# Optimization experiments

Measured on AMD Instinct MI355X. Metric: run time of the kernel, lower is better.

## Reference

```python
import jax, jax.numpy as jnp
import numpy as np

N_NODES = 100000
NEG_SLOPE = 0.01  # torch F.leaky_relu default

def _degrees(edge_src, edge_dst, n):
    ones = jnp.ones(edge_src.shape[0], dtype=jnp.float32)
    dout = jax.ops.segment_sum(ones, edge_src, num_segments=n)
    din = jax.ops.segment_sum(ones, edge_dst, num_segments=n)
    # DGL clamps zero degrees to 1 (norm='both')
    dout_inv_sqrt = jax.lax.rsqrt(jnp.maximum(dout, 1.0))
    din_inv_sqrt = jax.lax.rsqrt(jnp.maximum(din, 1.0))
    return dout_inv_sqrt, din_inv_sqrt

def _graph_conv(x, W, b, edge_src, edge_dst, dout_is, din_is, n):
    # DGL GraphConv, norm='both': h_i = b + sum_{j->i} (x_j W) / sqrt(d_out(j) d_in(i))
    h = (x * dout_is[:, None]) @ W            # [N, out]
    agg = jax.ops.segment_sum(h[edge_src], edge_dst, num_segments=n)
    return agg * din_is[:, None] + b

def setup_inputs() -> dict:
    key = jax.random.key(0)
    ks = jax.random.split(key, 16)
    n, e = N_NODES, 1600000
    features = jax.random.normal(ks[0], (n, 4), dtype=jnp.float32)
    edge_src = jax.random.randint(ks[1], (e,), 0, n, dtype=jnp.int32)
    edge_dst = jax.random.randint(ks[2], (e,), 0, n, dtype=jnp.int32)
    dims = [(4, 128), (128, 128), (128, 128), (128, 128), (128, 3)]
    inp = {"features": features, "edge_src": edge_src, "edge_dst": edge_dst}
    for i, (fi, fo) in enumerate(dims):
        s = (2.0 / (fi + fo)) ** 0.5  # glorot
        inp[f"W{i+1}"] = jax.random.normal(ks[3 + i], (fi, fo), dtype=jnp.float32) * s
        inp[f"b{i+1}"] = jnp.zeros((fo,), dtype=jnp.float32)
    return inp

def reference(features, edge_src, edge_dst, W1, b1, W2, b2, W3, b3, W4, b4, W5, b5):
    n = features.shape[0]
    dout_is, din_is = _degrees(edge_src, edge_dst, n)
    lrelu = lambda x: jnp.where(x >= 0, x, NEG_SLOPE * x)
    x = lrelu(_graph_conv(features, W1, b1, edge_src, edge_dst, dout_is, din_is, n))
    x = lrelu(_graph_conv(x, W2, b2, edge_src, edge_dst, dout_is, din_is, n))
    x = lrelu(_graph_conv(x, W3, b3, edge_src, edge_dst, dout_is, din_is, n))
    x = lrelu(_graph_conv(x, W4, b4, edge_src, edge_dst, dout_is, din_is, n))
    x = _graph_conv(x, W5, b5, edge_src, edge_dst, dout_is, din_is, n)
    return x
```

## Files before the change

### kernel.cpp

```cpp
#include <hip/hip_runtime.h>
#include <hip/hip_fp16.h>
#include <math.h>


#define LRELU_SLOPE 0.01f
#define XPAD 129
#define MAXBUCK 512


__device__ inline void chunk_range(int E, int nchunks, int cid, int& lo, int& hi) {
    int chunk = (E + nchunks - 1) / nchunks;
    lo = cid * chunk;
    hi = min(E, lo + chunk);
}

__global__ __launch_bounds__(256) void k_part_hist2(const int* __restrict__ src, const int* __restrict__ dst,
                                                    int E, int nbuck,
                                                    unsigned* __restrict__ gHistS, unsigned* __restrict__ gHistD,
                                                    unsigned* __restrict__ blockBaseS, unsigned* __restrict__ blockBaseD) {
    __shared__ unsigned hs[MAXBUCK];
    __shared__ unsigned hd[MAXBUCK];
    for (int i = threadIdx.x; i < nbuck; i += 256) { hs[i] = 0u; hd[i] = 0u; }
    __syncthreads();
    int lo, hi;
    chunk_range(E, gridDim.x, blockIdx.x, lo, hi);
    for (int e = lo + threadIdx.x; e < hi; e += 256) {
        atomicAdd(&hs[src[e] >> 8], 1u);
        atomicAdd(&hd[dst[e] >> 8], 1u);
    }
    __syncthreads();
    for (int i = threadIdx.x; i < nbuck; i += 256) {
        blockBaseS[(size_t)blockIdx.x * nbuck + i] = atomicAdd(&gHistS[i], hs[i]);
        blockBaseD[(size_t)blockIdx.x * nbuck + i] = atomicAdd(&gHistD[i], hd[i]);
    }
}

__global__ __launch_bounds__(512) void k_part_scan(const unsigned* __restrict__ gHist, int nbuck,
                                                   unsigned* __restrict__ bucketStart,
                                                   unsigned* __restrict__ row_ptr_last, unsigned Eval) {
    __shared__ unsigned s[MAXBUCK];
    int t = threadIdx.x;
    s[t] = (t < nbuck) ? gHist[t] : 0u;
    __syncthreads();
    for (int off = 1; off < MAXBUCK; off <<= 1) {
        unsigned v = (t >= off) ? s[t - off] : 0u;
        __syncthreads();
        s[t] += v;
        __syncthreads();
    }
    if (t <= nbuck) bucketStart[t] = (t == 0) ? 0u : s[t - 1];
    if (t == 0 && row_ptr_last) *row_ptr_last = Eval;
}

__global__ __launch_bounds__(256) void k_part_scatter_both(const int* __restrict__ src, const int* __restrict__ dst,
                                                           int E, int nbuck,
                                                           const unsigned* __restrict__ bstartS,
                                                           const unsigned* __restrict__ bstartD,
                                                           const unsigned* __restrict__ blockBaseS,
                                                           const unsigned* __restrict__ blockBaseD,
                                                           int2* __restrict__ pairs, int* __restrict__ srcbuf) {
    __shared__ unsigned curS[MAXBUCK];
    __shared__ unsigned curD[MAXBUCK];
    for (int i = threadIdx.x; i < nbuck; i += 256) {
        curS[i] = bstartS[i] + blockBaseS[(size_t)blockIdx.x * nbuck + i];
        curD[i] = bstartD[i] + blockBaseD[(size_t)blockIdx.x * nbuck + i];
    }
    __syncthreads();
    int lo, hi;
    chunk_range(E, gridDim.x, blockIdx.x, lo, hi);
    for (int e = lo + threadIdx.x; e < hi; e += 256) {
        int s = src[e], d = dst[e];
        unsigned posD = atomicAdd(&curD[d >> 8], 1u);
        pairs[posD] = make_int2(s, d);
        unsigned posS = atomicAdd(&curS[s >> 8], 1u);
        srcbuf[posS] = s;
    }
}

__global__ __launch_bounds__(256) void k_bucket_csr(const int2* __restrict__ pairs,
                                                    const unsigned* __restrict__ bucketStart,
                                                    unsigned* __restrict__ row_ptr,
                                                    unsigned* __restrict__ din_cnt,
                                                    int* __restrict__ csr, int n) {
    __shared__ unsigned hist[256];
    __shared__ unsigned scanw[256];
    __shared__ unsigned cur[256];
    int b = blockIdx.x, t = threadIdx.x;
    unsigned beg = bucketStart[b], end = bucketStart[b + 1];
    hist[t] = 0u;
    __syncthreads();
    for (unsigned e = beg + t; e < end; e += 256)
        atomicAdd(&hist[pairs[e].y & 255], 1u);
    __syncthreads();
    scanw[t] = hist[t];
    __syncthreads();
    for (int off = 1; off < 256; off <<= 1) {
        unsigned u = (t >= off) ? scanw[t - off] : 0u;
        __syncthreads();
        scanw[t] += u;
        __syncthreads();
    }
    unsigned excl = scanw[t] - hist[t];
    int node = (b << 8) + t;
    if (node < n) {
        row_ptr[node] = beg + excl;
        din_cnt[node] = hist[t];
    }
    cur[t] = excl;
    __syncthreads();
    for (unsigned e = beg + t; e < end; e += 256) {
        int2 p = pairs[e];
        unsigned pos = beg + atomicAdd(&cur[p.y & 255], 1u);
        csr[pos] = p.x;
    }
}

__global__ __launch_bounds__(256) void k_bucket_cnt(const int* __restrict__ vals,
                                                    const unsigned* __restrict__ bucketStart,
                                                    unsigned* __restrict__ dout_cnt, int n) {
    __shared__ unsigned hist[256];
    int b = blockIdx.x, t = threadIdx.x;
    unsigned beg = bucketStart[b], end = bucketStart[b + 1];
    hist[t] = 0u;
    __syncthreads();
    for (unsigned e = beg + t; e < end; e += 256)
        atomicAdd(&hist[vals[e] & 255], 1u);
    __syncthreads();
    int node = (b << 8) + t;
    if (node < n) dout_cnt[node] = hist[t];
}

__global__ void k_invsqrt2(const unsigned* __restrict__ c0, float* __restrict__ i0,
                           const unsigned* __restrict__ c1, float* __restrict__ i1, int n) {
    int i = blockIdx.x * blockDim.x + threadIdx.x;
    if (i < n) {
        i0[i] = 1.0f / sqrtf(fmaxf((float)c0[i], 1.0f));
        i1[i] = 1.0f / sqrtf(fmaxf((float)c1[i], 1.0f));
    }
}


__global__ void k_prescale4(const float* __restrict__ x, const float* __restrict__ dout_is,
                            float* __restrict__ pf4, int n) {
    int i = blockIdx.x * blockDim.x + threadIdx.x;
    if (i >= n) return;
    float s = dout_is[i];
    float4 v = *reinterpret_cast<const float4*>(x + (size_t)i * 4);
    float4 o = {v.x * s, v.y * s, v.z * s, v.w * s};
    *reinterpret_cast<float4*>(pf4 + (size_t)i * 4) = o;
}

__global__ void k_gather4(const float* __restrict__ pf4, const int* __restrict__ csr,
                          const unsigned* __restrict__ row_ptr, const float* __restrict__ din_is,
                          const float* __restrict__ dout_is, float* __restrict__ a4, int n) {
    int i = blockIdx.x * blockDim.x + threadIdx.x;
    if (i >= n) return;
    unsigned beg = row_ptr[i], end = row_ptr[i + 1];
    float4 acc = {0.f, 0.f, 0.f, 0.f};
    unsigned e = beg;
    for (; e + 4 <= end; e += 4) {
        int s0 = csr[e], s1 = csr[e + 1], s2 = csr[e + 2], s3 = csr[e + 3];
        float4 v0 = *reinterpret_cast<const float4*>(pf4 + (size_t)s0 * 4);
        float4 v1 = *reinterpret_cast<const float4*>(pf4 + (size_t)s1 * 4);
        float4 v2 = *reinterpret_cast<const float4*>(pf4 + (size_t)s2 * 4);
        float4 v3 = *reinterpret_cast<const float4*>(pf4 + (size_t)s3 * 4);
        acc.x += (v0.x + v1.x) + (v2.x + v3.x);
        acc.y += (v0.y + v1.y) + (v2.y + v3.y);
        acc.z += (v0.z + v1.z) + (v2.z + v3.z);
        acc.w += (v0.w + v1.w) + (v2.w + v3.w);
    }
    for (; e < end; ++e) {
        int s = csr[e];
        float4 v = *reinterpret_cast<const float4*>(pf4 + (size_t)s * 4);
        acc.x += v.x; acc.y += v.y; acc.z += v.z; acc.w += v.w;
    }
    float sc = din_is[i] * dout_is[i];
    float4 o = {acc.x * sc, acc.y * sc, acc.z * sc, acc.w * sc};
    *reinterpret_cast<float4*>(a4 + (size_t)i * 4) = o;
}


__device__ inline void sth16(__half* p, const float* v) {
    __half2 hh[8];
#pragma unroll
    for (int q = 0; q < 8; ++q) hh[q] = __floats2half2_rn(v[2 * q], v[2 * q + 1]);
    const float4* f = reinterpret_cast<const float4*>(&hh[0]);
    *reinterpret_cast<float4*>(p) = f[0];
    *reinterpret_cast<float4*>(p + 8) = f[1];
}

__device__ inline void acc8(float* acc, uint4 u) {
    const __half2* h = reinterpret_cast<const __half2*>(&u);
#pragma unroll
    for (int q = 0; q < 4; ++q) {
        float2 f = __half22float2(h[q]);
        acc[2 * q] += f.x;
        acc[2 * q + 1] += f.y;
    }
}


__device__ inline float4 xp1_cols(float4 av, float ds, float4 wa, float4 wb, float4 wc, float4 wd, float4 bc) {
    float4 r;
    r.x = fmaf(av.x, wa.x, fmaf(av.y, wb.x, fmaf(av.z, wc.x, fmaf(av.w, wd.x, ds * bc.x))));
    r.y = fmaf(av.x, wa.y, fmaf(av.y, wb.y, fmaf(av.z, wc.y, fmaf(av.w, wd.y, ds * bc.y))));
    r.z = fmaf(av.x, wa.z, fmaf(av.y, wb.z, fmaf(av.z, wc.z, fmaf(av.w, wd.z, ds * bc.z))));
    r.w = fmaf(av.x, wa.w, fmaf(av.y, wb.w, fmaf(av.z, wc.w, fmaf(av.w, wd.w, ds * bc.w))));
    r.x = fmaxf(r.x, LRELU_SLOPE * r.x);
    r.y = fmaxf(r.y, LRELU_SLOPE * r.y);
    r.z = fmaxf(r.z, LRELU_SLOPE * r.z);
    r.w = fmaxf(r.w, LRELU_SLOPE * r.w);
    return r;
}

__global__ __launch_bounds__(512) void k_gl12(const float* __restrict__ a4,
                                              const float* __restrict__ dout_v,
                                              const int* __restrict__ csr,
                                              const unsigned* __restrict__ row_ptr,
                                              const float* __restrict__ din_is, const float* __restrict__ dout_is,
                                              const float* __restrict__ W1, const float* __restrict__ b1,
                                              const float* __restrict__ W2, const float* __restrict__ b2,
                                              __half* __restrict__ xh_out, int n) {
    __shared__ float xs[64 * XPAD];
    const int t = threadIdx.x;
    const int bbase = blockIdx.x * 64;
    const int wave = t >> 6;
    const int lane = t & 63;
    const int half = lane >> 5;
    const int j4 = (lane & 31) * 4;

    float4 wa = *reinterpret_cast<const float4*>(W1 + 0 * 128 + j4);
    float4 wb = *reinterpret_cast<const float4*>(W1 + 1 * 128 + j4);
    float4 wc = *reinterpret_cast<const float4*>(W1 + 2 * 128 + j4);
    float4 wd = *reinterpret_cast<const float4*>(W1 + 3 * 128 + j4);
    float4 bc = *reinterpret_cast<const float4*>(b1 + j4);

#pragma unroll
    for (int sweep = 0; sweep < 4; ++sweep) {
        int r = wave * 2 + half + sweep * 16;
        int node = bbase + r;
        float4 acc = {0.f, 0.f, 0.f, 0.f};
        if (node < n) {
            unsigned beg = row_ptr[node], end = row_ptr[node + 1];
            unsigned e = beg;
            for (; e + 4 <= end; e += 4) {
                int s0 = csr[e + 0], s1 = csr[e + 1], s2 = csr[e + 2], s3 = csr[e + 3];
                float4 a0 = *reinterpret_cast<const float4*>(a4 + (size_t)s0 * 4);
                float4 a1 = *reinterpret_cast<const float4*>(a4 + (size_t)s1 * 4);
                float4 a2 = *reinterpret_cast<const float4*>(a4 + (size_t)s2 * 4);
                float4 a3 = *reinterpret_cast<const float4*>(a4 + (size_t)s3 * 4);
                float d0 = dout_v[s0], d1 = dout_v[s1], d2 = dout_v[s2], d3 = dout_v[s3];
                float4 x0 = xp1_cols(a0, d0, wa, wb, wc, wd, bc);
                float4 x1 = xp1_cols(a1, d1, wa, wb, wc, wd, bc);
                float4 x2 = xp1_cols(a2, d2, wa, wb, wc, wd, bc);
                float4 x3 = xp1_cols(a3, d3, wa, wb, wc, wd, bc);
                acc.x += (x0.x + x1.x) + (x2.x + x3.x);
                acc.y += (x0.y + x1.y) + (x2.y + x3.y);
                acc.z += (x0.z + x1.z) + (x2.z + x3.z);
                acc.w += (x0.w + x1.w) + (x2.w + x3.w);
            }
            for (; e < end; ++e) {
                int s = csr[e];
                float4 av = *reinterpret_cast<const float4*>(a4 + (size_t)s * 4);
                float4 xv = xp1_cols(av, dout_v[s], wa, wb, wc, wd, bc);
                acc.x += xv.x; acc.y += xv.y; acc.z += xv.z; acc.w += xv.w;
            }
            float di = din_is[node];
            acc.x *= di; acc.y *= di; acc.z *= di; acc.w *= di;
        }
        float* d = xs + r * XPAD + j4;
        d[0] = acc.x; d[1] = acc.y; d[2] = acc.z; d[3] = acc.w;
    }
    __syncthreads();

    const int jg = __builtin_amdgcn_readfirstlane(wave) & 7;
    const int j0 = jg * 16;
    const float* Wj = W2 + j0;
    const float* xrow = xs + lane * XPAD;

    float acc[16];
#pragma unroll
    for (int q = 0; q < 16; ++q) acc[q] = 0.f;

#pragma unroll 2
    for (int k = 0; k < 128; k += 4) {
        float x0 = xrow[k + 0];
        float x1 = xrow[k + 1];
        float x2 = xrow[k + 2];
        float x3 = xrow[k + 3];
        const float* w0 = Wj + (size_t)k * 128;
#pragma unroll
        for (int q = 0; q < 16; ++q) {
            acc[q] += x0 * w0[q] + x1 * w0[128 + q] + x2 * w0[256 + q] + x3 * w0[384 + q];
        }
    }

    int node = bbase + lane;
    if (node < n) {
        float s = dout_is[node];
        float v[16];
#pragma unroll
        for (int q = 0; q < 16; ++q) {
            float u = acc[q] + b2[j0 + q];
            u = fmaxf(u, LRELU_SLOPE * u);
            v[q] = u * s;
        }
        sth16(xh_out + (size_t)node * 128 + j0, v);
    }
}


#define GATHER_FP16_TILE(XH)                                                           \
    for (int sweep = 0; sweep < 8; ++sweep) {                                          \
        int r = sweep * 8 + wave;                                                      \
        int node = bbase + r;                                                          \
        float acc[8];                                                                  \
        _Pragma("unroll") for (int q = 0; q < 8; ++q) acc[q] = 0.f;                    \
        float di = 0.f;                                                                \
        if (node < n) {                                                                \
            unsigned beg = row_ptr[node], end = row_ptr[node + 1];                     \
            unsigned e = beg;                                                          \
            for (; e + 16 <= end; e += 16) {                                           \
                int s0 = csr[e + 0 + sub2];                                            \
                int s1 = csr[e + 4 + sub2];                                            \
                int s2 = csr[e + 8 + sub2];                                            \
                int s3 = csr[e + 12 + sub2];                                           \
                uint4 u0 = *reinterpret_cast<const uint4*>(XH + (size_t)s0 * 128 + c8); \
                uint4 u1 = *reinterpret_cast<const uint4*>(XH + (size_t)s1 * 128 + c8); \
                uint4 u2 = *reinterpret_cast<const uint4*>(XH + (size_t)s2 * 128 + c8); \
                uint4 u3 = *reinterpret_cast<const uint4*>(XH + (size_t)s3 * 128 + c8); \
                acc8(acc, u0); acc8(acc, u1); acc8(acc, u2); acc8(acc, u3);            \
            }                                                                          \
            for (; e + 4 <= end; e += 4) {                                             \
                int s = csr[e + sub2];                                                 \
                acc8(acc, *reinterpret_cast<const uint4*>(XH + (size_t)s * 128 + c8)); \
            }                                                                          \
            int rem = (int)(end - e);                                                  \
            if (sub2 < rem) {                                                          \
                int s = csr[e + sub2];                                                 \
                acc8(acc, *reinterpret_cast<const uint4*>(XH + (size_t)s * 128 + c8)); \
            }                                                                          \
            di = din_is[node];                                                         \
        }                                                                              \
        _Pragma("unroll") for (int q = 0; q < 8; ++q) {                                \
            acc[q] += __shfl_xor(acc[q], 16, 64);                                      \
            acc[q] += __shfl_xor(acc[q], 32, 64);                                      \
        }                                                                              \
        if (sub2 == 0) {                                                               \
            float* d = xs + r * XPAD + c8;                                             \
            _Pragma("unroll") for (int q = 0; q < 8; ++q) d[q] = acc[q] * di;          \
        }                                                                              \
    }


__global__ __launch_bounds__(512) void k_gl128h(const __half* __restrict__ xh, const int* __restrict__ csr,
                                                const unsigned* __restrict__ row_ptr,
                                                const float* __restrict__ din_is, const float* __restrict__ dout_is,
                                                const float* __restrict__ W, const float* __restrict__ b,
                                                __half* __restrict__ xh_out, int n) {
    __shared__ float xs[64 * XPAD];
    const int t = threadIdx.x;
    const int bbase = blockIdx.x * 64;
    const int wave = t >> 6;
    const int lane = t & 63;
    const int sub2 = lane >> 4;
    const int c8 = (lane & 15) * 8;

    GATHER_FP16_TILE(xh)
    __syncthreads();

    const int jg = __builtin_amdgcn_readfirstlane(wave) & 7;
    const int j0 = jg * 16;
    const float* Wj = W + j0;
    const float* xrow = xs + lane * XPAD;

    float acc[16];
#pragma unroll
    for (int q = 0; q < 16; ++q) acc[q] = 0.f;

#pragma unroll 2
    for (int k = 0; k < 128; k += 4) {
        float x0 = xrow[k + 0];
        float x1 = xrow[k + 1];
        float x2 = xrow[k + 2];
        float x3 = xrow[k + 3];
        const float* w0 = Wj + (size_t)k * 128;
#pragma unroll
        for (int q = 0; q < 16; ++q) {
            acc[q] += x0 * w0[q] + x1 * w0[128 + q] + x2 * w0[256 + q] + x3 * w0[384 + q];
        }
    }

    int node = bbase + lane;
    if (node < n) {
        float s = dout_is[node];
        float v[16];
#pragma unroll
        for (int q = 0; q < 16; ++q) {
            float u = acc[q] + b[j0 + q];
            u = fmaxf(u, LRELU_SLOPE * u);
            v[q] = u * s;
        }
        sth16(xh_out + (size_t)node * 128 + j0, v);
    }
}


__global__ __launch_bounds__(512) void k_gl128f(const __half* __restrict__ xh, const int* __restrict__ csr,
                                                const unsigned* __restrict__ row_ptr,
                                                const float* __restrict__ din_is, const float* __restrict__ dout_is,
                                                const float* __restrict__ W, const float* __restrict__ b,
                                                const float* __restrict__ W5,
                                                float* __restrict__ h5, int n) {
    __shared__ float xs[64 * XPAD];
    const int t = threadIdx.x;
    const int bbase = blockIdx.x * 64;
    const int wave = t >> 6;
    const int lane = t & 63;
    const int sub2 = lane >> 4;
    const int c8 = (lane & 15) * 8;

    GATHER_FP16_TILE(xh)
    __syncthreads();

    const int jg = __builtin_amdgcn_readfirstlane(wave) & 7;
    const int j0 = jg * 16;
    const float* Wj = W + j0;
    const float* xrow = xs + lane * XPAD;

    float acc[16];
#pragma unroll
    for (int q = 0; q < 16; ++q) acc[q] = 0.f;

#pragma unroll 2
    for (int k = 0; k < 128; k += 4) {
        float x0 = xrow[k + 0];
        float x1 = xrow[k + 1];
        float x2 = xrow[k + 2];
        float x3 = xrow[k + 3];
        const float* w0 = Wj + (size_t)k * 128;
#pragma unroll
        for (int q = 0; q < 16; ++q) {
            acc[q] += x0 * w0[q] + x1 * w0[128 + q] + x2 * w0[256 + q] + x3 * w0[384 + q];
        }
    }

    float s = (bbase + lane < n) ? dout_is[bbase + lane] : 0.f;
    float p0 = 0.f, p1 = 0.f, p2 = 0.f;
#pragma unroll
    for (int q = 0; q < 16; ++q) {
        float u = acc[q] + b[j0 + q];
        u = fmaxf(u, LRELU_SLOPE * u);
        u *= s;
        const float* w5r = W5 + (size_t)(j0 + q) * 3;
        p0 = fmaf(u, w5r[0], p0);
        p1 = fmaf(u, w5r[1], p1);
        p2 = fmaf(u, w5r[2], p2);
    }
    __syncthreads();
    float* red = xs;
    red[lane * 24 + wave * 3 + 0] = p0;
    red[lane * 24 + wave * 3 + 1] = p1;
    red[lane * 24 + wave * 3 + 2] = p2;
    __syncthreads();
    if (t < 64) {
        int node = bbase + t;
        if (node < n) {
            float a0 = 0.f, a1 = 0.f, a2 = 0.f;
#pragma unroll
            for (int w = 0; w < 8; ++w) {
                a0 += red[t * 24 + w * 3 + 0];
                a1 += red[t * 24 + w * 3 + 1];
                a2 += red[t * 24 + w * 3 + 2];
            }
            h5[(size_t)node * 3 + 0] = a0;
            h5[(size_t)node * 3 + 1] = a1;
            h5[(size_t)node * 3 + 2] = a2;
        }
    }
}


__global__ void k_gather3(const float* __restrict__ h, const int* __restrict__ csr,
                          const unsigned* __restrict__ row_ptr, const float* __restrict__ din_is,
                          const float* __restrict__ b, float* __restrict__ out, int n) {
    int i = blockIdx.x * blockDim.x + threadIdx.x;
    if (i >= n) return;
    unsigned beg = row_ptr[i], end = row_ptr[i + 1];
    float a0 = 0.f, a1 = 0.f, a2 = 0.f;
    for (unsigned e = beg; e < end; ++e) {
        int s = csr[e];
        a0 += h[(size_t)s * 3 + 0];
        a1 += h[(size_t)s * 3 + 1];
        a2 += h[(size_t)s * 3 + 2];
    }
    float di = din_is[i];
    out[(size_t)i * 3 + 0] = a0 * di + b[0];
    out[(size_t)i * 3 + 1] = a1 * di + b[1];
    out[(size_t)i * 3 + 2] = a2 * di + b[2];
}


extern "C" void kernel_launch(void* const* d_in, const int* in_sizes, int n_in,
                              void* d_out, int out_size, void* d_ws, size_t ws_size,
                              hipStream_t stream) {
    const float* features = (const float*)d_in[0];
    const int* esrc = (const int*)d_in[1];
    const int* edst = (const int*)d_in[2];
    const float* W1 = (const float*)d_in[3];  const float* b1 = (const float*)d_in[4];
    const float* W2 = (const float*)d_in[5];  const float* b2 = (const float*)d_in[6];
    const float* W3 = (const float*)d_in[7];  const float* b3 = (const float*)d_in[8];
    const float* W4 = (const float*)d_in[9];  const float* b4 = (const float*)d_in[10];
    const float* W5 = (const float*)d_in[11]; const float* b5 = (const float*)d_in[12];

    const int N = in_sizes[0] / 4;
    const int E = in_sizes[1];
    const int nbuck = (N + 255) / 256;
    const int NPB = 256;

    size_t off = 0;
    auto carve = [&](size_t bytes) -> void* {
        void* p = (char*)d_ws + off;
        off = (off + bytes + 255) & ~(size_t)255;
        return p;
    };
    char*     scratch   = (char*)carve((size_t)E * 12 + 256);
    float*    Bp        = (float*)carve((size_t)N * 8 * 4);
    __half*   xh2       = (__half*)carve((size_t)N * 128 * 2);
    __half*   xh3       = (__half*)carve((size_t)N * 128 * 2);
    int*      csr       = (int*)carve((size_t)E * 4);
    unsigned* row_ptr   = (unsigned*)carve((size_t)(N + 1) * 4);
    unsigned* dout_cnt  = (unsigned*)carve((size_t)N * 4);
    unsigned* din_cnt   = (unsigned*)carve((size_t)N * 4);
    float*    dout_is   = (float*)carve((size_t)N * 4);
    float*    din_is    = (float*)carve((size_t)N * 4);
    unsigned* gHistD    = (unsigned*)carve((size_t)MAXBUCK * 4);
    unsigned* gHistS    = (unsigned*)carve((size_t)MAXBUCK * 4);
    unsigned* bstartD   = (unsigned*)carve((size_t)(MAXBUCK + 1) * 4);
    unsigned* bstartS   = (unsigned*)carve((size_t)(MAXBUCK + 1) * 4);
    unsigned* blockBaseD = (unsigned*)carve((size_t)NPB * nbuck * 4);
    unsigned* blockBaseS = (unsigned*)carve((size_t)NPB * nbuck * 4);
    float*    h5        = (float*)carve((size_t)N * 3 * 4);
    (void)ws_size;
    int2* pairs  = (int2*)scratch;
    int*  srcbuf = (int*)(scratch + (size_t)E * 8);
    float* pf4 = Bp;
    float* a4  = Bp + (size_t)N * 4;

    hipMemsetAsync(gHistD, 0, (size_t)MAXBUCK * 4, stream);
    hipMemsetAsync(gHistS, 0, (size_t)MAXBUCK * 4, stream);

    k_part_hist2<<<NPB, 256, 0, stream>>>(esrc, edst, E, nbuck, gHistS, gHistD, blockBaseS, blockBaseD);
    k_part_scan<<<1, 512, 0, stream>>>(gHistD, nbuck, bstartD, row_ptr + N, (unsigned)E);
    k_part_scan<<<1, 512, 0, stream>>>(gHistS, nbuck, bstartS, (unsigned*)nullptr, 0u);
    k_part_scatter_both<<<NPB, 256, 0, stream>>>(esrc, edst, E, nbuck, bstartS, bstartD,
                                                 blockBaseS, blockBaseD, pairs, srcbuf);
    k_bucket_csr<<<nbuck, 256, 0, stream>>>(pairs, bstartD, row_ptr, din_cnt, csr, N);
    k_bucket_cnt<<<nbuck, 256, 0, stream>>>(srcbuf, bstartS, dout_cnt, N);
    k_invsqrt2<<<(N + 255) / 256, 256, 0, stream>>>(dout_cnt, dout_is, din_cnt, din_is, N);

    k_prescale4<<<(N + 255) / 256, 256, 0, stream>>>(features, dout_is, pf4, N);
    k_gather4<<<(N + 255) / 256, 256, 0, stream>>>(pf4, csr, row_ptr, din_is, dout_is, a4, N);

    int glGrid = (N + 63) / 64;
    k_gl12<<<glGrid, 512, 0, stream>>>(a4, dout_is, csr, row_ptr, din_is, dout_is, W1, b1, W2, b2, xh2, N);
    k_gl128h<<<glGrid, 512, 0, stream>>>(xh2, csr, row_ptr, din_is, dout_is, W3, b3, xh3, N);
    k_gl128f<<<glGrid, 512, 0, stream>>>(xh3, csr, row_ptr, din_is, dout_is, W4, b4, W5, h5, N);

    k_gather3<<<(N + 255) / 256, 256, 0, stream>>>(h5, csr, row_ptr, din_is, b5, (float*)d_out, N);
}
```

Before: 451.4 us.

## Split fused gather+GEMM layers into column-sliced gather and separate linear kernels

```diff
diff --git a/kernel.cpp b/kernel.cpp
--- a/kernel.cpp
+++ b/kernel.cpp
@@ -189,14 +189,29 @@
     *reinterpret_cast<float4*>(p + 8) = f[1];
 }
 
-__device__ inline void acc8(float* acc, uint4 u) {
-    const __half2* h = reinterpret_cast<const __half2*>(&u);
-#pragma unroll
-    for (int q = 0; q < 4; ++q) {
-        float2 f = __half22float2(h[q]);
-        acc[2 * q] += f.x;
-        acc[2 * q + 1] += f.y;
-    }
+__device__ inline float2 h2f(unsigned u) {
+    __half2 h = *reinterpret_cast<__half2*>(&u);
+    return __half22float2(h);
+}
+
+__device__ inline int degree_rank_row(const unsigned* __restrict__ row_ptr,
+                                      int bbase, int lane, int n) {
+    int node0 = bbase + lane;
+    int deg = 0;
+    if (node0 < n) deg = (int)(row_ptr[node0 + 1] - row_ptr[node0]);
+    int key = (deg << 8) | lane;
+#pragma unroll
+    for (int k = 2; k <= 64; k <<= 1) {
+#pragma unroll
+        for (int j = k >> 1; j >= 1; j >>= 1) {
+            int other = __shfl_xor(key, j, 64);
+            bool up = ((lane & k) == 0);
+            bool lower = ((lane & j) == 0);
+            int mn = min(key, other), mx = max(key, other);
+            key = (up == lower) ? mn : mx;
+        }
+    }
+    return key & 255;
 }
 
 
@@ -310,65 +325,96 @@
 }
 
 
-#define GATHER_FP16_TILE(XH)                                                           \
-    for (int sweep = 0; sweep < 8; ++sweep) {                                          \
-        int r = sweep * 8 + wave;                                                      \
-        int node = bbase + r;                                                          \
-        float acc[8];                                                                  \
-        _Pragma("unroll") for (int q = 0; q < 8; ++q) acc[q] = 0.f;                    \
-        float di = 0.f;                                                                \
-        if (node < n) {                                                                \
-            unsigned beg = row_ptr[node], end = row_ptr[node + 1];                     \
-            unsigned e = beg;                                                          \
-            for (; e + 16 <= end; e += 16) {                                           \
-                int s0 = csr[e + 0 + sub2];                                            \
-                int s1 = csr[e + 4 + sub2];                                            \
-                int s2 = csr[e + 8 + sub2];                                            \
-                int s3 = csr[e + 12 + sub2];                                           \
-                uint4 u0 = *reinterpret_cast<const uint4*>(XH + (size_t)s0 * 128 + c8); \
-                uint4 u1 = *reinterpret_cast<const uint4*>(XH + (size_t)s1 * 128 + c8); \
-                uint4 u2 = *reinterpret_cast<const uint4*>(XH + (size_t)s2 * 128 + c8); \
-                uint4 u3 = *reinterpret_cast<const uint4*>(XH + (size_t)s3 * 128 + c8); \
-                acc8(acc, u0); acc8(acc, u1); acc8(acc, u2); acc8(acc, u3);            \
-            }                                                                          \
-            for (; e + 4 <= end; e += 4) {                                             \
-                int s = csr[e + sub2];                                                 \
-                acc8(acc, *reinterpret_cast<const uint4*>(XH + (size_t)s * 128 + c8)); \
-            }                                                                          \
-            int rem = (int)(end - e);                                                  \
-            if (sub2 < rem) {                                                          \
-                int s = csr[e + sub2];                                                 \
-                acc8(acc, *reinterpret_cast<const uint4*>(XH + (size_t)s * 128 + c8)); \
-            }                                                                          \
-            di = din_is[node];                                                         \
-        }                                                                              \
-        _Pragma("unroll") for (int q = 0; q < 8; ++q) {                                \
-            acc[q] += __shfl_xor(acc[q], 16, 64);                                      \
-            acc[q] += __shfl_xor(acc[q], 32, 64);                                      \
-        }                                                                              \
-        if (sub2 == 0) {                                                               \
-            float* d = xs + r * XPAD + c8;                                             \
-            _Pragma("unroll") for (int q = 0; q < 8; ++q) d[q] = acc[q] * di;          \
-        }                                                                              \
-    }
-
-
-__global__ __launch_bounds__(512) void k_gl128h(const __half* __restrict__ xh, const int* __restrict__ csr,
-                                                const unsigned* __restrict__ row_ptr,
-                                                const float* __restrict__ din_is, const float* __restrict__ dout_is,
-                                                const float* __restrict__ W, const float* __restrict__ b,
-                                                __half* __restrict__ xh_out, int n) {
+__global__ __launch_bounds__(256) void k_gcol(const __half* __restrict__ xh, const int* __restrict__ csr,
+                                              const unsigned* __restrict__ row_ptr,
+                                              const float* __restrict__ din_is,
+                                              __half* __restrict__ g, int n) {
+    const int slice = blockIdx.x & 7;
+    const int bbase = (blockIdx.x >> 3) * 64;
+    const int t = threadIdx.x;
+    const int wave = t >> 6;
+    const int lane = t & 63;
+    const int grp = lane >> 3;
+    const int li = lane & 7;
+    const int c0 = slice * 16 + li * 2;
+
+    const int Lr = degree_rank_row(row_ptr, bbase, lane, n);
+
+#pragma unroll
+    for (int sweep = 0; sweep < 2; ++sweep) {
+        int rank = sweep * 32 + wave * 8 + grp;
+        int r = __shfl(Lr, rank, 64);
+        int node = bbase + r;
+        float a0 = 0.f, a1 = 0.f;
+        float b0 = 0.f, b1 = 0.f;
+        if (node < n) {
+            unsigned beg = row_ptr[node], end = row_ptr[node + 1];
+            unsigned e = beg;
+            for (; e + 8 <= end; e += 8) {
+                int s0 = csr[e + 0], s1 = csr[e + 1], s2 = csr[e + 2], s3 = csr[e + 3];
+                int s4 = csr[e + 4], s5 = csr[e + 5], s6 = csr[e + 6], s7 = csr[e + 7];
+                unsigned u0 = *reinterpret_cast<const unsigned*>(xh + (size_t)s0 * 128 + c0);
+                unsigned u1 = *reinterpret_cast<const unsigned*>(xh + (size_t)s1 * 128 + c0);
+                unsigned u2 = *reinterpret_cast<const unsigned*>(xh + (size_t)s2 * 128 + c0);
+                unsigned u3 = *reinterpret_cast<const unsigned*>(xh + (size_t)s3 * 128 + c0);
+                unsigned u4 = *reinterpret_cast<const unsigned*>(xh + (size_t)s4 * 128 + c0);
+                unsigned u5 = *reinterpret_cast<const unsigned*>(xh + (size_t)s5 * 128 + c0);
+                unsigned u6 = *reinterpret_cast<const unsigned*>(xh + (size_t)s6 * 128 + c0);
+                unsigned u7 = *reinterpret_cast<const unsigned*>(xh + (size_t)s7 * 128 + c0);
+                float2 f0 = h2f(u0), f1 = h2f(u1), f2 = h2f(u2), f3 = h2f(u3);
+                float2 f4 = h2f(u4), f5 = h2f(u5), f6 = h2f(u6), f7 = h2f(u7);
+                a0 += (f0.x + f1.x) + (f2.x + f3.x);
+                a1 += (f0.y + f1.y) + (f2.y + f3.y);
+                b0 += (f4.x + f5.x) + (f6.x + f7.x);
+                b1 += (f4.y + f5.y) + (f6.y + f7.y);
+            }
+            for (; e < end; ++e) {
+                int s = csr[e];
+                float2 f = h2f(*reinterpret_cast<const unsigned*>(xh + (size_t)s * 128 + c0));
+                a0 += f.x; a1 += f.y;
+            }
+            float di = din_is[node];
+            a0 = (a0 + b0) * di;
+            a1 = (a1 + b1) * di;
+            __half2 o = __floats2half2_rn(a0, a1);
+            *reinterpret_cast<__half2*>(g + (size_t)node * 128 + c0) = o;
+        }
+    }
+}
+
+
+__global__ __launch_bounds__(512) void k_lin128g(const __half* __restrict__ g,
+                                                 const float* __restrict__ dout_is,
+                                                 const float* __restrict__ W, const float* __restrict__ b,
+                                                 __half* __restrict__ xh_out, int n) {
     __shared__ float xs[64 * XPAD];
     const int t = threadIdx.x;
     const int bbase = blockIdx.x * 64;
+    {
+        int node = bbase + (t >> 3);
+        int c = (t & 7) * 16;
+        float v[16];
+        if (node < n) {
+            uint4 u0 = *reinterpret_cast<const uint4*>(g + (size_t)node * 128 + c);
+            uint4 u1 = *reinterpret_cast<const uint4*>(g + (size_t)node * 128 + c + 8);
+            const unsigned* uu = reinterpret_cast<const unsigned*>(&u0);
+#pragma unroll
+            for (int q = 0; q < 4; ++q) { float2 f = h2f(uu[q]); v[2 * q] = f.x; v[2 * q + 1] = f.y; }
+            uu = reinterpret_cast<const unsigned*>(&u1);
+#pragma unroll
+            for (int q = 0; q < 4; ++q) { float2 f = h2f(uu[q]); v[8 + 2 * q] = f.x; v[9 + 2 * q] = f.y; }
+        } else {
+#pragma unroll
+            for (int q = 0; q < 16; ++q) v[q] = 0.f;
+        }
+        float* d = xs + (t >> 3) * XPAD + c;
+#pragma unroll
+        for (int q = 0; q < 16; ++q) d[q] = v[q];
+    }
+    __syncthreads();
+
     const int wave = t >> 6;
     const int lane = t & 63;
-    const int sub2 = lane >> 4;
-    const int c8 = (lane & 15) * 8;
-
-    GATHER_FP16_TILE(xh)
-    __syncthreads();
-
     const int jg = __builtin_amdgcn_readfirstlane(wave) & 7;
     const int j0 = jg * 16;
     const float* Wj = W + j0;
@@ -406,23 +452,39 @@
 }
 
 
-__global__ __launch_bounds__(512) void k_gl128f(const __half* __restrict__ xh, const int* __restrict__ csr,
-                                                const unsigned* __restrict__ row_ptr,
-                                                const float* __restrict__ din_is, const float* __restrict__ dout_is,
-                                                const float* __restrict__ W, const float* __restrict__ b,
-                                                const float* __restrict__ W5,
-                                                float* __restrict__ h5, int n) {
+__global__ __launch_bounds__(512) void k_lin128g5(const __half* __restrict__ g,
+                                                  const float* __restrict__ dout_is,
+                                                  const float* __restrict__ W, const float* __restrict__ b,
+                                                  const float* __restrict__ W5,
+                                                  float* __restrict__ h5, int n) {
     __shared__ float xs[64 * XPAD];
     const int t = threadIdx.x;
     const int bbase = blockIdx.x * 64;
+    {
+        int node = bbase + (t >> 3);
+        int c = (t & 7) * 16;
+        float v[16];
+        if (node < n) {
+            uint4 u0 = *reinterpret_cast<const uint4*>(g + (size_t)node * 128 + c);
+            uint4 u1 = *reinterpret_cast<const uint4*>(g + (size_t)node * 128 + c + 8);
+            const unsigned* uu = reinterpret_cast<const unsigned*>(&u0);
+#pragma unroll
+            for (int q = 0; q < 4; ++q) { float2 f = h2f(uu[q]); v[2 * q] = f.x; v[2 * q + 1] = f.y; }
+            uu = reinterpret_cast<const unsigned*>(&u1);
+#pragma unroll
+            for (int q = 0; q < 4; ++q) { float2 f = h2f(uu[q]); v[8 + 2 * q] = f.x; v[9 + 2 * q] = f.y; }
+        } else {
+#pragma unroll
+            for (int q = 0; q < 16; ++q) v[q] = 0.f;
+        }
+        float* d = xs + (t >> 3) * XPAD + c;
+#pragma unroll
+        for (int q = 0; q < 16; ++q) d[q] = v[q];
+    }
+    __syncthreads();
+
     const int wave = t >> 6;
     const int lane = t & 63;
-    const int sub2 = lane >> 4;
-    const int c8 = (lane & 15) * 8;
-
-    GATHER_FP16_TILE(xh)
-    __syncthreads();
-
     const int jg = __builtin_amdgcn_readfirstlane(wave) & 7;
     const int j0 = jg * 16;
     const float* Wj = W + j0;
@@ -528,6 +590,7 @@
     float*    Bp        = (float*)carve((size_t)N * 8 * 4);
     __half*   xh2       = (__half*)carve((size_t)N * 128 * 2);
     __half*   xh3       = (__half*)carve((size_t)N * 128 * 2);
+    __half*   gbuf      = (__half*)carve((size_t)N * 128 * 2);
     int*      csr       = (int*)carve((size_t)E * 4);
     unsigned* row_ptr   = (unsigned*)carve((size_t)(N + 1) * 4);
     unsigned* dout_cnt  = (unsigned*)carve((size_t)N * 4);
@@ -562,10 +625,14 @@
     k_prescale4<<<(N + 255) / 256, 256, 0, stream>>>(features, dout_is, pf4, N);
     k_gather4<<<(N + 255) / 256, 256, 0, stream>>>(pf4, csr, row_ptr, din_is, dout_is, a4, N);
 
-    int glGrid = (N + 63) / 64;
-    k_gl12<<<glGrid, 512, 0, stream>>>(a4, dout_is, csr, row_ptr, din_is, dout_is, W1, b1, W2, b2, xh2, N);
-    k_gl128h<<<glGrid, 512, 0, stream>>>(xh2, csr, row_ptr, din_is, dout_is, W3, b3, xh3, N);
-    k_gl128f<<<glGrid, 512, 0, stream>>>(xh3, csr, row_ptr, din_is, dout_is, W4, b4, W5, h5, N);
+    int nTiles = (N + 63) / 64;
+    k_gl12<<<nTiles, 512, 0, stream>>>(a4, dout_is, csr, row_ptr, din_is, dout_is, W1, b1, W2, b2, xh2, N);
+
+    k_gcol<<<nTiles * 8, 256, 0, stream>>>(xh2, csr, row_ptr, din_is, gbuf, N);
+    k_lin128g<<<nTiles, 512, 0, stream>>>(gbuf, dout_is, W3, b3, xh3, N);
+
+    k_gcol<<<nTiles * 8, 256, 0, stream>>>(xh3, csr, row_ptr, din_is, gbuf, N);
+    k_lin128g5<<<nTiles, 512, 0, stream>>>(gbuf, dout_is, W4, b4, W5, h5, N);
 
     k_gather3<<<(N + 255) / 256, 256, 0, stream>>>(h5, csr, row_ptr, din_is, b5, (float*)d_out, N);
 }
```

After: 710.6 us. 57.4% more time.
